# Optimization experiments

Hardware: AMD Instinct MI355X
Metric: run time of the kernel (lower is better)

Reference implementation:

```python
import jax, jax.numpy as jnp
import numpy as np

N = 200000   # nodes
E = 600000   # directed edges
G = 8192     # graphs in batch
D_IN = 30
H = 128


def setup_inputs() -> dict:
    key = jax.random.key(0)
    ks = jax.random.split(key, 9)
    x = jax.random.normal(ks[0], (N, D_IN), jnp.float32)
    edge_index = jax.random.randint(ks[1], (2, E), 0, N, dtype=jnp.int32)
    batch_idx = jnp.sort(jax.random.randint(ks[2], (N,), 0, G, dtype=jnp.int32))
    W1 = jax.random.normal(ks[3], (D_IN, H), jnp.float32) / np.sqrt(D_IN)
    b1 = jnp.zeros((H,), jnp.float32)
    W2 = jax.random.normal(ks[4], (H, H), jnp.float32) / np.sqrt(H)
    b2 = jnp.zeros((H,), jnp.float32)
    W3 = jax.random.normal(ks[5], (H, H), jnp.float32) / np.sqrt(H)
    b3 = jnp.zeros((H,), jnp.float32)
    return {"x": x, "edge_index": edge_index, "batch_idx": batch_idx,
            "W1": W1, "b1": b1, "W2": W2, "b2": b2, "W3": W3, "b3": b3}


def _gcn_layer(x, W, b, src, dst, dinv):
    h = x @ W                                   # [N, H]
    norm = (dinv[src] * dinv[dst])[:, None]     # per-edge normalization
    msg = h[src] * norm                         # [E, H] gather + scale
    agg = jax.ops.segment_sum(msg, dst, num_segments=N)
    agg = agg + h * (dinv * dinv)[:, None]      # self-loop term, norm = 1/deg
    return jax.nn.relu(agg + b)


def reference(x, edge_index, batch_idx, W1, b1, W2, b2, W3, b3):
    src, dst = edge_index[0], edge_index[1]
    # degree with self-loops (edge weight 1), aggregated at target (col)
    deg = 1.0 + jax.ops.segment_sum(jnp.ones((E,), x.dtype), dst, num_segments=N)
    dinv = jax.lax.rsqrt(deg)                   # deg >= 1, safe
    h = _gcn_layer(x, W1, b1, src, dst, dinv)
    h = _gcn_layer(h, W2, b2, src, dst, dinv)
    h = _gcn_layer(h, W3, b3, src, dst, dinv)
    # global mean pool over batch segments
    sums = jax.ops.segment_sum(h, batch_idx, num_segments=G)
    counts = jax.ops.segment_sum(jnp.ones((N,), h.dtype), batch_idx, num_segments=G)
    return sums / jnp.maximum(counts, 1.0)[:, None]
```

## Files before the change

kernel.cpp:

```cpp
#include <hip/hip_runtime.h>


#define DIN 30
#define HD  128

typedef __attribute__((ext_vector_type(8))) short v8s;
typedef __attribute__((ext_vector_type(4))) float v4f;

static __device__ __forceinline__ unsigned short f2bf(float f) {
  unsigned int u = __float_as_uint(f);
  u += 0x7fffu + ((u >> 16) & 1u);
  return (unsigned short)(u >> 16);
}
static __device__ __forceinline__ float bf2f(unsigned short s) {
  return __uint_as_float(((unsigned int)s) << 16);
}
static __device__ __forceinline__ float bflo(unsigned int u) {
  return __uint_as_float(u << 16);
}
static __device__ __forceinline__ float bfhi(unsigned int u) {
  return __uint_as_float(u & 0xffff0000u);
}

#define ACC8(v, s)                                            \
  {                                                           \
    a0 += (s) * (float)((v).x & 0xffu);                       \
    a1 += (s) * (float)(((v).x >> 8) & 0xffu);                \
    a2 += (s) * (float)(((v).x >> 16) & 0xffu);               \
    a3 += (s) * (float)((v).x >> 24);                         \
    a4 += (s) * (float)((v).y & 0xffu);                       \
    a5 += (s) * (float)(((v).y >> 8) & 0xffu);                \
    a6 += (s) * (float)(((v).y >> 16) & 0xffu);               \
    a7 += (s) * (float)((v).y >> 24);                         \
  }

__global__ void k_degree(const int* __restrict__ dst, int* __restrict__ deg,
                         int* __restrict__ eord, int E) {
  int e = blockIdx.x * blockDim.x + threadIdx.x;
  if (e < E) eord[e] = atomicAdd(&deg[dst[e]], 1);
}

__global__ void k_scan(const int* __restrict__ deg, int* __restrict__ scanbuf,
                       int* __restrict__ rowptr, float* __restrict__ dinv, int N) {
  __shared__ int s[256];
  __shared__ int sbase;
  int bid = blockIdx.x, tid = threadIdx.x;
  int base = bid * 1024 + tid * 4;
  int v[4]; int t = 0;
#pragma unroll
  for (int j = 0; j < 4; ++j) { int idx = base + j; v[j] = (idx < N) ? deg[idx] : 0; t += v[j]; }
  s[tid] = t; __syncthreads();
  for (int d = 1; d < 256; d <<= 1) {
    int u = (tid >= d) ? s[tid - d] : 0;
    __syncthreads();
    s[tid] += u;
    __syncthreads();
  }
  int myexcl = s[tid] - t;
  int blocktotal = s[255];
  if (tid == 0) atomicExch(&scanbuf[bid], blocktotal | 0x80000000);

  int pre = 0;
  for (int p = tid; p < bid; p += 256) {
    int val;
    do { val = atomicAdd(&scanbuf[p], 0); } while (!(val & 0x80000000));
    pre += val & 0x7fffffff;
  }
  __syncthreads();
  s[tid] = pre; __syncthreads();
  for (int d = 128; d > 0; d >>= 1) { if (tid < d) s[tid] += s[tid + d]; __syncthreads(); }
  if (tid == 0) sbase = s[0];
  __syncthreads();

  int run = sbase + myexcl;
#pragma unroll
  for (int j = 0; j < 4; ++j) {
    int idx = base + j;
    if (idx < N) {
      rowptr[idx] = run;
      dinv[idx] = rsqrtf((float)(1 + v[j]));
    }
    run += v[j];
    if (idx == N - 1) rowptr[N] = run;
  }
}

static __device__ __forceinline__ void wtf_one(const float* __restrict__ W,
                                               unsigned short* __restrict__ WTF,
                                               int idx, int Kreal, int KK) {
  int j = idx & 7;
  int c = idx >> 3;
  int l15 = c & 15;
  int quad = (c >> 4) & 3;
  int kk = (c >> 6) % KK;
  int t = c / (64 * KK);
  int k = kk * 32 + quad * 8 + j;
  int n = t * 16 + l15;
  WTF[idx] = (k < Kreal) ? f2bf(W[k * 128 + n]) : (unsigned short)0;
}

__global__ void k_prep(const int* __restrict__ src, const int* __restrict__ dst,
                       const int* __restrict__ rowptr, const int* __restrict__ eord,
                       int* __restrict__ col, int E,
                       const float* __restrict__ x, const float* __restrict__ dinv,
                       unsigned short* __restrict__ xb, int N,
                       const float* __restrict__ W1, const float* __restrict__ W2,
                       const float* __restrict__ W3,
                       unsigned short* __restrict__ W1F, unsigned short* __restrict__ W2F,
                       unsigned short* __restrict__ W3F,
                       const int* __restrict__ batch, int* __restrict__ gstart, int G,
                       float* __restrict__ out,
                       int SB, int XB, int WB, int BB) {
  int blk = blockIdx.x;
  if (blk < SB) {
    int e = blk * 256 + threadIdx.x;
    if (e < E) col[rowptr[dst[e]] + eord[e]] = src[e];
  } else if (blk < SB + XB) {
    int idx = (blk - SB) * 256 + threadIdx.x;
    if (idx < N * 32) {
      int n = idx >> 5, f = idx & 31;
      float v = (f < DIN) ? x[(size_t)n * DIN + f] * dinv[n] : 0.f;
      xb[idx] = f2bf(v);
    }
  } else if (blk < SB + XB + WB) {
    int idx = (blk - SB - XB) * 256 + threadIdx.x;
    if (idx < 4096) wtf_one(W1, W1F, idx, DIN, 1);
    else if (idx < 20480) wtf_one(W2, W2F, idx - 4096, 128, 4);
    else if (idx < 36864) wtf_one(W3, W3F, idx - 20480, 128, 4);
  } else if (blk < SB + XB + WB + BB) {
    int i = (blk - SB - XB - WB) * 256 + threadIdx.x;
    if (i >= N) return;
    int b = batch[i];
    int prev = (i == 0) ? -1 : batch[i - 1];
    for (int g = prev + 1; g <= b; ++g) gstart[g] = i;
    if (i == N - 1)
      for (int g = b + 1; g <= G; ++g) gstart[g] = N;
  } else {
    int idx = (blk - SB - XB - WB - BB) * 256 + threadIdx.x;
    if (idx < G * 32)
      ((float4*)out)[idx] = make_float4(0.f, 0.f, 0.f, 0.f);
  }
}

template <int K>
__global__ __launch_bounds__(1024, 8) void k_fused(const void* __restrict__ hin,
                                                   const float* __restrict__ hscale,
                                                   const unsigned short* __restrict__ WTF,
                                                   const float* __restrict__ b,
                                                   const int* __restrict__ rowptr,
                                                   const int* __restrict__ col,
                                                   const float* __restrict__ dinv,
                                                   unsigned char* __restrict__ Cq,
                                                   float* __restrict__ Cs, int N) {
  constexpr int KK = K / 32;
  constexpr int KP = (K == 128) ? 136 : 40;
  constexpr int CP = 132;
  constexpr int SMSZ = (64 * KP > 64 * CP) ? 64 * KP : 64 * CP;
  __shared__ __align__(16) unsigned short sm[SMSZ];

  int tid = threadIdx.x;
  int l16 = tid & 15;
  int nl = tid >> 4;
  int row0 = blockIdx.x * 64;
  int node = row0 + nl;

  if constexpr (K == 32) {
    const unsigned int* hp = (const unsigned int*)hin;
    float a0 = 0.f, a1 = 0.f;
    if (node < N) {
      unsigned int u = hp[(size_t)node * 16 + l16];
      a0 = bflo(u); a1 = bfhi(u);
      int e0 = rowptr[node], e1 = rowptr[node + 1];
      int e = e0;
      for (; e + 2 <= e1; e += 2) {
        int c0 = col[e], c1 = col[e + 1];
        unsigned int v0 = hp[(size_t)c0 * 16 + l16];
        unsigned int v1 = hp[(size_t)c1 * 16 + l16];
        a0 += bflo(v0); a1 += bfhi(v0);
        a0 += bflo(v1); a1 += bfhi(v1);
      }
      if (e < e1) {
        unsigned int v0 = hp[(size_t)col[e] * 16 + l16];
        a0 += bflo(v0); a1 += bfhi(v0);
      }
      float di = dinv[node];
      a0 *= di; a1 *= di;
    }
    *(unsigned int*)&sm[nl * KP + l16 * 2] =
        (unsigned int)f2bf(a0) | ((unsigned int)f2bf(a1) << 16);
  } else {
    const uint2* hq = (const uint2*)hin;
    float a0 = 0.f, a1 = 0.f, a2 = 0.f, a3 = 0.f, a4 = 0.f, a5 = 0.f, a6 = 0.f, a7 = 0.f;
    if (node < N) {
      uint2 u = hq[(size_t)node * 16 + l16];
      float ss = hscale[node];
      ACC8(u, ss);
      int e0 = rowptr[node], e1 = rowptr[node + 1];
      int e = e0;
      for (; e + 2 <= e1; e += 2) {
        int c0 = col[e], c1 = col[e + 1];
        uint2 v0 = hq[(size_t)c0 * 16 + l16];
        uint2 v1 = hq[(size_t)c1 * 16 + l16];
        float s0 = hscale[c0];
        float s1 = hscale[c1];
        ACC8(v0, s0);
        ACC8(v1, s1);
      }
      if (e < e1) {
        int c0 = col[e];
        uint2 v0 = hq[(size_t)c0 * 16 + l16];
        float s0 = hscale[c0];
        ACC8(v0, s0);
      }
      float di = dinv[node];
      a0 *= di; a1 *= di; a2 *= di; a3 *= di;
      a4 *= di; a5 *= di; a6 *= di; a7 *= di;
    }
    uint4 o;
    o.x = (unsigned int)f2bf(a0) | ((unsigned int)f2bf(a1) << 16);
    o.y = (unsigned int)f2bf(a2) | ((unsigned int)f2bf(a3) << 16);
    o.z = (unsigned int)f2bf(a4) | ((unsigned int)f2bf(a5) << 16);
    o.w = (unsigned int)f2bf(a6) | ((unsigned int)f2bf(a7) << 16);
    *(uint4*)&sm[nl * KP + l16 * 8] = o;
  }
  __syncthreads();

  int wv = tid >> 6, lane = tid & 63, quad = lane >> 4, l15 = lane & 15;
  int rt = wv & 3, tp = wv >> 2;
  v8s af[KK];
#pragma unroll
  for (int kk = 0; kk < KK; ++kk)
    af[kk] = *(const v8s*)&sm[(rt * 16 + l15) * KP + kk * 32 + quad * 8];
  __syncthreads();

  int crow0 = row0 + rt * 16 + quad * 4;
  float dr[4];
  if (crow0 + 3 < N) {
    float4 d4 = *(const float4*)&dinv[crow0];
    dr[0] = d4.x; dr[1] = d4.y; dr[2] = d4.z; dr[3] = d4.w;
  } else {
#pragma unroll
    for (int i = 0; i < 4; ++i) dr[i] = (crow0 + i < N) ? dinv[crow0 + i] : 0.f;
  }

#pragma unroll
  for (int tt = 0; tt < 2; ++tt) {
    int t = tp * 2 + tt;
    v4f acc = {0.f, 0.f, 0.f, 0.f};
#pragma unroll
    for (int kk = 0; kk < KK; ++kk) {
      v8s bf = *(const v8s*)(WTF + (size_t)(((t * KK + kk) * 4 + quad) * 16 + l15) * 8);
      acc = __builtin_amdgcn_mfma_f32_16x16x32_bf16(af[kk], bf, acc, 0, 0, 0);
    }
    float bias = b[t * 16 + l15];
#pragma unroll
    for (int i = 0; i < 4; ++i) {
      float o = fmaxf(acc[i] + bias, 0.f) * dr[i];
      sm[(rt * 16 + quad * 4 + i) * CP + t * 16 + l15] = f2bf(o);
    }
  }
  __syncthreads();

  {
    uint4 u = *(const uint4*)&sm[nl * CP + l16 * 8];
    float f0 = bflo(u.x), f1 = bfhi(u.x), f2 = bflo(u.y), f3 = bfhi(u.y);
    float f4 = bflo(u.z), f5 = bfhi(u.z), f6 = bflo(u.w), f7 = bfhi(u.w);
    float m = fmaxf(fmaxf(fmaxf(f0, f1), fmaxf(f2, f3)),
                    fmaxf(fmaxf(f4, f5), fmaxf(f6, f7)));
    m = fmaxf(m, __shfl_xor(m, 1));
    m = fmaxf(m, __shfl_xor(m, 2));
    m = fmaxf(m, __shfl_xor(m, 4));
    m = fmaxf(m, __shfl_xor(m, 8));
    float inv = (m > 0.f) ? 255.f / m : 0.f;
    unsigned q0 = (unsigned)__float2int_rn(fminf(f0 * inv, 255.f));
    unsigned q1 = (unsigned)__float2int_rn(fminf(f1 * inv, 255.f));
    unsigned q2 = (unsigned)__float2int_rn(fminf(f2 * inv, 255.f));
    unsigned q3 = (unsigned)__float2int_rn(fminf(f3 * inv, 255.f));
    unsigned q4 = (unsigned)__float2int_rn(fminf(f4 * inv, 255.f));
    unsigned q5 = (unsigned)__float2int_rn(fminf(f5 * inv, 255.f));
    unsigned q6 = (unsigned)__float2int_rn(fminf(f6 * inv, 255.f));
    unsigned q7 = (unsigned)__float2int_rn(fminf(f7 * inv, 255.f));
    uint2 o;
    o.x = q0 | (q1 << 8) | (q2 << 16) | (q3 << 24);
    o.y = q4 | (q5 << 8) | (q6 << 16) | (q7 << 24);
    int row = row0 + nl;
    if (row < N) {
      ((uint2*)Cq)[(size_t)row * 16 + l16] = o;
      if (l16 == 0) Cs[row] = m * (1.f / 255.f);
    }
  }
}

__global__ __launch_bounds__(1024, 8) void k_fused_pool(const unsigned char* __restrict__ hin,
                                                        const float* __restrict__ hscale,
                                                        const unsigned short* __restrict__ WTF,
                                                        const float* __restrict__ b,
                                                        const int* __restrict__ rowptr,
                                                        const int* __restrict__ col,
                                                        const float* __restrict__ dinv,
                                                        const int* __restrict__ batch,
                                                        float* __restrict__ out, int N) {
  constexpr int KK = 4, KP = 136, CP = 132;
  constexpr int SMSZ = 64 * KP;
  __shared__ __align__(16) unsigned short sm[SMSZ];
  __shared__ int sbatch[64];

  int tid = threadIdx.x;
  int l16 = tid & 15;
  int nl = tid >> 4;
  int row0 = blockIdx.x * 64;
  int node = row0 + nl;

  if (tid < 64) sbatch[tid] = (row0 + tid < N) ? batch[row0 + tid] : -1;

  {
    const uint2* hq = (const uint2*)hin;
    float a0 = 0.f, a1 = 0.f, a2 = 0.f, a3 = 0.f, a4 = 0.f, a5 = 0.f, a6 = 0.f, a7 = 0.f;
    if (node < N) {
      uint2 u = hq[(size_t)node * 16 + l16];
      float ss = hscale[node];
      ACC8(u, ss);
      int e0 = rowptr[node], e1 = rowptr[node + 1];
      int e = e0;
      for (; e + 2 <= e1; e += 2) {
        int c0 = col[e], c1 = col[e + 1];
        uint2 v0 = hq[(size_t)c0 * 16 + l16];
        uint2 v1 = hq[(size_t)c1 * 16 + l16];
        float s0 = hscale[c0];
        float s1 = hscale[c1];
        ACC8(v0, s0);
        ACC8(v1, s1);
      }
      if (e < e1) {
        int c0 = col[e];
        uint2 v0 = hq[(size_t)c0 * 16 + l16];
        float s0 = hscale[c0];
        ACC8(v0, s0);
      }
      float di = dinv[node];
      a0 *= di; a1 *= di; a2 *= di; a3 *= di;
      a4 *= di; a5 *= di; a6 *= di; a7 *= di;
    }
    uint4 o;
    o.x = (unsigned int)f2bf(a0) | ((unsigned int)f2bf(a1) << 16);
    o.y = (unsigned int)f2bf(a2) | ((unsigned int)f2bf(a3) << 16);
    o.z = (unsigned int)f2bf(a4) | ((unsigned int)f2bf(a5) << 16);
    o.w = (unsigned int)f2bf(a6) | ((unsigned int)f2bf(a7) << 16);
    *(uint4*)&sm[nl * KP + l16 * 8] = o;
  }
  __syncthreads();

  int wv = tid >> 6, lane = tid & 63, quad = lane >> 4, l15 = lane & 15;
  int rt = wv & 3, tp = wv >> 2;
  v8s af[KK];
#pragma unroll
  for (int kk = 0; kk < KK; ++kk)
    af[kk] = *(const v8s*)&sm[(rt * 16 + l15) * KP + kk * 32 + quad * 8];
  __syncthreads();

#pragma unroll
  for (int tt = 0; tt < 2; ++tt) {
    int t = tp * 2 + tt;
    v4f acc = {0.f, 0.f, 0.f, 0.f};
#pragma unroll
    for (int kk = 0; kk < KK; ++kk) {
      v8s bf = *(const v8s*)(WTF + (size_t)(((t * KK + kk) * 4 + quad) * 16 + l15) * 8);
      acc = __builtin_amdgcn_mfma_f32_16x16x32_bf16(af[kk], bf, acc, 0, 0, 0);
    }
    float bias = b[t * 16 + l15];
#pragma unroll
    for (int i = 0; i < 4; ++i) {
      float o = fmaxf(acc[i] + bias, 0.f);
      sm[(rt * 16 + quad * 4 + i) * CP + t * 16 + l15] = f2bf(o);
    }
  }
  __syncthreads();

  int f = tid & 127;
  int grp = tid >> 7;
  float run = 0.f;
  int cur = -1;
#pragma unroll
  for (int j = 0; j < 8; ++j) {
    int r = grp * 8 + j;
    int g = sbatch[r];
    if (g != cur) {
      if (cur >= 0) atomicAdd(&out[(size_t)cur * 128 + f], run);
      run = 0.f; cur = g;
    }
    if (g >= 0) run += bf2f(sm[r * CP + f]);
  }
  if (cur >= 0) atomicAdd(&out[(size_t)cur * 128 + f], run);
}

__global__ void k_finalize(float* __restrict__ out, const int* __restrict__ gstart, int G) {
  int idx = blockIdx.x * blockDim.x + threadIdx.x;
  if (idx >= G * 128) return;
  int g = idx >> 7;
  float cnt = (float)(gstart[g + 1] - gstart[g]);
  out[idx] = out[idx] / fmaxf(cnt, 1.f);
}

extern "C" void kernel_launch(void* const* d_in, const int* in_sizes, int n_in,
                              void* d_out, int out_size, void* d_ws, size_t ws_size,
                              hipStream_t stream) {
  const float* x  = (const float*)d_in[0];
  const int* ei   = (const int*)d_in[1];
  const int* batch = (const int*)d_in[2];
  const float* W1 = (const float*)d_in[3];
  const float* b1 = (const float*)d_in[4];
  const float* W2 = (const float*)d_in[5];
  const float* b2 = (const float*)d_in[6];
  const float* W3 = (const float*)d_in[7];
  const float* b3 = (const float*)d_in[8];
  float* out = (float*)d_out;
  int N = in_sizes[2];
  int E = in_sizes[1] / 2;
  int G = out_size / HD;
  const int* src = ei;
  const int* dst = ei + E;

  size_t off = 0;
  char* ws = (char*)d_ws;
  auto alloc = [&](size_t bytes) -> void* {
    void* p = ws + off;
    off += (bytes + 255) & ~(size_t)255;
    return p;
  };
  int nb1024 = (N + 1023) / 1024;
  int*   deg     = (int*)alloc((size_t)N * 4);
  int*   scanbuf = (int*)alloc((size_t)nb1024 * 4);
  float* dinv    = (float*)alloc((size_t)N * 4);
  int*   rowptr  = (int*)alloc((size_t)(N + 1) * 4);
  int*   eord    = (int*)alloc((size_t)E * 4);
  int*   col     = (int*)alloc((size_t)E * 4);
  int*   gstart  = (int*)alloc((size_t)(G + 1) * 4);
  unsigned short* xb  = (unsigned short*)alloc((size_t)N * 32 * 2);
  unsigned char*  hAq = (unsigned char*)alloc((size_t)N * 128);
  float*          hAs = (float*)alloc((size_t)N * 4);
  unsigned char*  hBq = (unsigned char*)alloc((size_t)N * 128);
  float*          hBs = (float*)alloc((size_t)N * 4);
  unsigned short* W1F = (unsigned short*)alloc(4096 * 2);
  unsigned short* W2F = (unsigned short*)alloc(16384 * 2);
  unsigned short* W3F = (unsigned short*)alloc(16384 * 2);
  (void)ws_size; (void)n_in;

  size_t zbytes = (size_t)((char*)dinv - (char*)deg);
  hipMemsetAsync(deg, 0, zbytes, stream);
  k_degree<<<(E + 255) / 256, 256, 0, stream>>>(dst, deg, eord, E);
  k_scan<<<nb1024, 256, 0, stream>>>(deg, scanbuf, rowptr, dinv, N);

  int SB = (E + 255) / 256;
  int XB = (N * 32 + 255) / 256;
  int WB = 144;
  int BB = (N + 255) / 256;
  int ZB = (G * 32 + 255) / 256;
  k_prep<<<SB + XB + WB + BB + ZB, 256, 0, stream>>>(src, dst, rowptr, eord, col, E,
                                                     x, dinv, xb, N,
                                                     W1, W2, W3, W1F, W2F, W3F,
                                                     batch, gstart, G, out,
                                                     SB, XB, WB, BB);

  int fusedBlocks = (N + 63) / 64;
  k_fused<32><<<fusedBlocks, 1024, 0, stream>>>(xb, nullptr, W1F, b1, rowptr, col, dinv,
                                                hAq, hAs, N);
  k_fused<128><<<fusedBlocks, 1024, 0, stream>>>(hAq, hAs, W2F, b2, rowptr, col, dinv,
                                                 hBq, hBs, N);
  k_fused_pool<<<fusedBlocks, 1024, 0, stream>>>(hBq, hBs, W3F, b3, rowptr, col, dinv,
                                                 batch, out, N);
  k_finalize<<<(G * 128 + 255) / 256, 256, 0, stream>>>(out, gstart, G);
}
```

Measured before the change: 295.1 us.

## Parallelize neighbor aggregation over block edges with LDS float atomics

Replaces the per-node serial CSR gather loop with a block-wide edge-parallel scheme. Each 64-node block walks its contiguous edge range 256 edges at a time and accumulates into an fp32 LDS tile with shared-memory atomics, using the local destination row packed into the top bits of col. The aim is to balance work across skewed degrees and raise memory-level parallelism. The cost is LDS atomic traffic, a larger fp32 shared tile that may lower occupancy, and the packing caps node ids at 18 bits (mask 0x3ffff = 262143), which only holds while N stays below that.

```diff
diff --git a/kernel.cpp b/kernel.cpp
--- a/kernel.cpp
+++ b/kernel.cpp
@@ -21,18 +21,6 @@
 static __device__ __forceinline__ float bfhi(unsigned int u) {
   return __uint_as_float(u & 0xffff0000u);
 }
-
-#define ACC8(v, s)                                            \
-  {                                                           \
-    a0 += (s) * (float)((v).x & 0xffu);                       \
-    a1 += (s) * (float)(((v).x >> 8) & 0xffu);                \
-    a2 += (s) * (float)(((v).x >> 16) & 0xffu);               \
-    a3 += (s) * (float)((v).x >> 24);                         \
-    a4 += (s) * (float)((v).y & 0xffu);                       \
-    a5 += (s) * (float)(((v).y >> 8) & 0xffu);                \
-    a6 += (s) * (float)(((v).y >> 16) & 0xffu);               \
-    a7 += (s) * (float)((v).y >> 24);                         \
-  }
 
 __global__ void k_degree(const int* __restrict__ dst, int* __restrict__ deg,
                          int* __restrict__ eord, int E) {
@@ -101,9 +89,9 @@
 
 __global__ void k_prep(const int* __restrict__ src, const int* __restrict__ dst,
                        const int* __restrict__ rowptr, const int* __restrict__ eord,
-                       int* __restrict__ col, int E,
+                       unsigned int* __restrict__ col, int E,
                        const float* __restrict__ x, const float* __restrict__ dinv,
-                       unsigned short* __restrict__ xb, int N,
+                       unsigned int* __restrict__ xb, int N,
                        const float* __restrict__ W1, const float* __restrict__ W2,
                        const float* __restrict__ W3,
                        unsigned short* __restrict__ W1F, unsigned short* __restrict__ W2F,
@@ -114,13 +102,18 @@
   int blk = blockIdx.x;
   if (blk < SB) {
     int e = blk * 256 + threadIdx.x;
-    if (e < E) col[rowptr[dst[e]] + eord[e]] = src[e];
+    if (e < E) {
+      int d = dst[e];
+      col[rowptr[d] + eord[e]] = (unsigned int)src[e] | ((unsigned int)(d & 63) << 26);
+    }
   } else if (blk < SB + XB) {
     int idx = (blk - SB) * 256 + threadIdx.x;
-    if (idx < N * 32) {
-      int n = idx >> 5, f = idx & 31;
-      float v = (f < DIN) ? x[(size_t)n * DIN + f] * dinv[n] : 0.f;
-      xb[idx] = f2bf(v);
+    if (idx < N * 16) {
+      int n = idx >> 4, w = idx & 15;
+      float di = dinv[n];
+      float v0 = x[(size_t)n * DIN + w] * di;
+      float v1 = (w + 16 < DIN) ? x[(size_t)n * DIN + w + 16] * di : 0.f;
+      xb[idx] = (unsigned int)f2bf(v0) | ((unsigned int)f2bf(v1) << 16);
     }
   } else if (blk < SB + XB + WB) {
     int idx = (blk - SB - XB) * 256 + threadIdx.x;
@@ -148,90 +141,124 @@
                                                    const unsigned short* __restrict__ WTF,
                                                    const float* __restrict__ b,
                                                    const int* __restrict__ rowptr,
-                                                   const int* __restrict__ col,
+                                                   const unsigned int* __restrict__ col,
                                                    const float* __restrict__ dinv,
                                                    unsigned char* __restrict__ Cq,
                                                    float* __restrict__ Cs, int N) {
   constexpr int KK = K / 32;
-  constexpr int KP = (K == 128) ? 136 : 40;
+  constexpr int AST = (K == 128) ? 132 : 36;
   constexpr int CP = 132;
-  constexpr int SMSZ = (64 * KP > 64 * CP) ? 64 * KP : 64 * CP;
-  __shared__ __align__(16) unsigned short sm[SMSZ];
+  constexpr int SMB = (64 * AST * 4 > 64 * CP * 2) ? 64 * AST * 4 : 64 * CP * 2;
+  __shared__ __align__(16) char smraw[SMB];
+  float* accf = (float*)smraw;
+  unsigned short* smc = (unsigned short*)smraw;
 
   int tid = threadIdx.x;
   int l16 = tid & 15;
-  int nl = tid >> 4;
+  int g = tid >> 4;
   int row0 = blockIdx.x * 64;
-  int node = row0 + nl;
+  int node = row0 + g;
 
   if constexpr (K == 32) {
-    const unsigned int* hp = (const unsigned int*)hin;
-    float a0 = 0.f, a1 = 0.f;
+    const unsigned int* xp = (const unsigned int*)hin;
     if (node < N) {
-      unsigned int u = hp[(size_t)node * 16 + l16];
-      a0 = bflo(u); a1 = bfhi(u);
-      int e0 = rowptr[node], e1 = rowptr[node + 1];
-      int e = e0;
-      for (; e + 2 <= e1; e += 2) {
-        int c0 = col[e], c1 = col[e + 1];
-        unsigned int v0 = hp[(size_t)c0 * 16 + l16];
-        unsigned int v1 = hp[(size_t)c1 * 16 + l16];
-        a0 += bflo(v0); a1 += bfhi(v0);
-        a0 += bflo(v1); a1 += bfhi(v1);
-      }
-      if (e < e1) {
-        unsigned int v0 = hp[(size_t)col[e] * 16 + l16];
-        a0 += bflo(v0); a1 += bfhi(v0);
-      }
-      float di = dinv[node];
-      a0 *= di; a1 *= di;
-    }
-    *(unsigned int*)&sm[nl * KP + l16 * 2] =
-        (unsigned int)f2bf(a0) | ((unsigned int)f2bf(a1) << 16);
+      unsigned int xw = xp[(size_t)node * 16 + l16];
+      accf[g * AST + l16]      = bflo(xw);
+      accf[g * AST + 16 + l16] = bfhi(xw);
+    } else {
+      accf[g * AST + l16]      = 0.f;
+      accf[g * AST + 16 + l16] = 0.f;
+    }
   } else {
     const uint2* hq = (const uint2*)hin;
-    float a0 = 0.f, a1 = 0.f, a2 = 0.f, a3 = 0.f, a4 = 0.f, a5 = 0.f, a6 = 0.f, a7 = 0.f;
     if (node < N) {
       uint2 u = hq[(size_t)node * 16 + l16];
-      float ss = hscale[node];
-      ACC8(u, ss);
-      int e0 = rowptr[node], e1 = rowptr[node + 1];
-      int e = e0;
-      for (; e + 2 <= e1; e += 2) {
-        int c0 = col[e], c1 = col[e + 1];
-        uint2 v0 = hq[(size_t)c0 * 16 + l16];
-        uint2 v1 = hq[(size_t)c1 * 16 + l16];
-        float s0 = hscale[c0];
-        float s1 = hscale[c1];
-        ACC8(v0, s0);
-        ACC8(v1, s1);
+      float s = hscale[node];
+      accf[g * AST + 0 * 16 + l16] = s * (float)(u.x & 0xffu);
+      accf[g * AST + 1 * 16 + l16] = s * (float)((u.x >> 8) & 0xffu);
+      accf[g * AST + 2 * 16 + l16] = s * (float)((u.x >> 16) & 0xffu);
+      accf[g * AST + 3 * 16 + l16] = s * (float)(u.x >> 24);
+      accf[g * AST + 4 * 16 + l16] = s * (float)(u.y & 0xffu);
+      accf[g * AST + 5 * 16 + l16] = s * (float)((u.y >> 8) & 0xffu);
+      accf[g * AST + 6 * 16 + l16] = s * (float)((u.y >> 16) & 0xffu);
+      accf[g * AST + 7 * 16 + l16] = s * (float)(u.y >> 24);
+    } else {
+#pragma unroll
+      for (int j = 0; j < 8; ++j) accf[g * AST + j * 16 + l16] = 0.f;
+    }
+  }
+  __syncthreads();
+
+  {
+    int rend = row0 + 64; if (rend > N) rend = N;
+    int eb = rowptr[row0];
+    int ee = rowptr[rend];
+    for (int b0 = eb; b0 < ee; b0 += 256) {
+      int e0 = b0 + g * 4;
+      unsigned int pc[4];
+      uint2 rv[4];
+      unsigned int xv[4];
+      float sc[4];
+#pragma unroll
+      for (int s = 0; s < 4; ++s) {
+        int e = e0 + s;
+        pc[s] = (e < ee) ? col[e] : 0xffffffffu;
       }
-      if (e < e1) {
-        int c0 = col[e];
-        uint2 v0 = hq[(size_t)c0 * 16 + l16];
-        float s0 = hscale[c0];
-        ACC8(v0, s0);
+#pragma unroll
+      for (int s = 0; s < 4; ++s) {
+        if (pc[s] != 0xffffffffu) {
+          unsigned int c = pc[s] & 0x3ffffu;
+          if constexpr (K == 32) {
+            xv[s] = ((const unsigned int*)hin)[(size_t)c * 16 + l16];
+          } else {
+            rv[s] = ((const uint2*)hin)[(size_t)c * 16 + l16];
+            sc[s] = hscale[c];
+          }
+        }
       }
-      float di = dinv[node];
-      a0 *= di; a1 *= di; a2 *= di; a3 *= di;
-      a4 *= di; a5 *= di; a6 *= di; a7 *= di;
-    }
-    uint4 o;
-    o.x = (unsigned int)f2bf(a0) | ((unsigned int)f2bf(a1) << 16);
-    o.y = (unsigned int)f2bf(a2) | ((unsigned int)f2bf(a3) << 16);
-    o.z = (unsigned int)f2bf(a4) | ((unsigned int)f2bf(a5) << 16);
-    o.w = (unsigned int)f2bf(a6) | ((unsigned int)f2bf(a7) << 16);
-    *(uint4*)&sm[nl * KP + l16 * 8] = o;
+#pragma unroll
+      for (int s = 0; s < 4; ++s) {
+        if (pc[s] != 0xffffffffu) {
+          int d = (int)(pc[s] >> 26);
+          if constexpr (K == 32) {
+            atomicAdd(&accf[d * AST + l16], bflo(xv[s]));
+            atomicAdd(&accf[d * AST + 16 + l16], bfhi(xv[s]));
+          } else {
+            float s0 = sc[s];
+            atomicAdd(&accf[d * AST + 0 * 16 + l16], s0 * (float)(rv[s].x & 0xffu));
+            atomicAdd(&accf[d * AST + 1 * 16 + l16], s0 * (float)((rv[s].x >> 8) & 0xffu));
+            atomicAdd(&accf[d * AST + 2 * 16 + l16], s0 * (float)((rv[s].x >> 16) & 0xffu));
+            atomicAdd(&accf[d * AST + 3 * 16 + l16], s0 * (float)(rv[s].x >> 24));
+            atomicAdd(&accf[d * AST + 4 * 16 + l16], s0 * (float)(rv[s].y & 0xffu));
+            atomicAdd(&accf[d * AST + 5 * 16 + l16], s0 * (float)((rv[s].y >> 8) & 0xffu));
+            atomicAdd(&accf[d * AST + 6 * 16 + l16], s0 * (float)((rv[s].y >> 16) & 0xffu));
+            atomicAdd(&accf[d * AST + 7 * 16 + l16], s0 * (float)(rv[s].y >> 24));
+          }
+        }
+      }
+    }
   }
   __syncthreads();
 
   int wv = tid >> 6, lane = tid & 63, quad = lane >> 4, l15 = lane & 15;
   int rt = wv & 3, tp = wv >> 2;
+  int arow = rt * 16 + l15;
+  float dn = (row0 + arow < N) ? dinv[row0 + arow] : 0.f;
   v8s af[KK];
 #pragma unroll
-  for (int kk = 0; kk < KK; ++kk)
-    af[kk] = *(const v8s*)&sm[(rt * 16 + l15) * KP + kk * 32 + quad * 8];
-  __syncthreads();
+  for (int kk = 0; kk < KK; ++kk) {
+    const float* p = &accf[arow * AST + kk * 32 + quad * 8];
+    float4 x0 = *(const float4*)p;
+    float4 x1 = *(const float4*)(p + 4);
+    af[kk][0] = (short)f2bf(x0.x * dn);
+    af[kk][1] = (short)f2bf(x0.y * dn);
+    af[kk][2] = (short)f2bf(x0.z * dn);
+    af[kk][3] = (short)f2bf(x0.w * dn);
+    af[kk][4] = (short)f2bf(x1.x * dn);
+    af[kk][5] = (short)f2bf(x1.y * dn);
+    af[kk][6] = (short)f2bf(x1.z * dn);
+    af[kk][7] = (short)f2bf(x1.w * dn);
+  }
 
   int crow0 = row0 + rt * 16 + quad * 4;
   float dr[4];
@@ -242,6 +269,7 @@
 #pragma unroll
     for (int i = 0; i < 4; ++i) dr[i] = (crow0 + i < N) ? dinv[crow0 + i] : 0.f;
   }
+  __syncthreads();
 
 #pragma unroll
   for (int tt = 0; tt < 2; ++tt) {
@@ -256,34 +284,30 @@
 #pragma unroll
     for (int i = 0; i < 4; ++i) {
       float o = fmaxf(acc[i] + bias, 0.f) * dr[i];
-      sm[(rt * 16 + quad * 4 + i) * CP + t * 16 + l15] = f2bf(o);
+      smc[(rt * 16 + quad * 4 + i) * CP + t * 16 + l15] = f2bf(o);
     }
   }
   __syncthreads();
 
   {
-    uint4 u = *(const uint4*)&sm[nl * CP + l16 * 8];
-    float f0 = bflo(u.x), f1 = bfhi(u.x), f2 = bflo(u.y), f3 = bfhi(u.y);
-    float f4 = bflo(u.z), f5 = bfhi(u.z), f6 = bflo(u.w), f7 = bfhi(u.w);
-    float m = fmaxf(fmaxf(fmaxf(f0, f1), fmaxf(f2, f3)),
-                    fmaxf(fmaxf(f4, f5), fmaxf(f6, f7)));
+    float f[8];
+#pragma unroll
+    for (int j = 0; j < 8; ++j) f[j] = bf2f(smc[g * CP + j * 16 + l16]);
+    float m = fmaxf(fmaxf(fmaxf(f[0], f[1]), fmaxf(f[2], f[3])),
+                    fmaxf(fmaxf(f[4], f[5]), fmaxf(f[6], f[7])));
     m = fmaxf(m, __shfl_xor(m, 1));
     m = fmaxf(m, __shfl_xor(m, 2));
     m = fmaxf(m, __shfl_xor(m, 4));
     m = fmaxf(m, __shfl_xor(m, 8));
     float inv = (m > 0.f) ? 255.f / m : 0.f;
-    unsigned q0 = (unsigned)__float2int_rn(fminf(f0 * inv, 255.f));
-    unsigned q1 = (unsigned)__float2int_rn(fminf(f1 * inv, 255.f));
-    unsigned q2 = (unsigned)__float2int_rn(fminf(f2 * inv, 255.f));
-    unsigned q3 = (unsigned)__float2int_rn(fminf(f3 * inv, 255.f));
-    unsigned q4 = (unsigned)__float2int_rn(fminf(f4 * inv, 255.f));
-    unsigned q5 = (unsigned)__float2int_rn(fminf(f5 * inv, 255.f));
-    unsigned q6 = (unsigned)__float2int_rn(fminf(f6 * inv, 255.f));
-    unsigned q7 = (unsigned)__float2int_rn(fminf(f7 * inv, 255.f));
+    unsigned q[8];
+#pragma unroll
+    for (int j = 0; j < 8; ++j)
+      q[j] = (unsigned)__float2int_rn(fminf(f[j] * inv, 255.f));
     uint2 o;
-    o.x = q0 | (q1 << 8) | (q2 << 16) | (q3 << 24);
-    o.y = q4 | (q5 << 8) | (q6 << 16) | (q7 << 24);
-    int row = row0 + nl;
+    o.x = q[0] | (q[1] << 8) | (q[2] << 16) | (q[3] << 24);
+    o.y = q[4] | (q[5] << 8) | (q[6] << 16) | (q[7] << 24);
+    int row = row0 + g;
     if (row < N) {
       ((uint2*)Cq)[(size_t)row * 16 + l16] = o;
       if (l16 == 0) Cs[row] = m * (1.f / 255.f);
@@ -296,66 +320,106 @@
                                                         const unsigned short* __restrict__ WTF,
                                                         const float* __restrict__ b,
                                                         const int* __restrict__ rowptr,
-                                                        const int* __restrict__ col,
+                                                        const unsigned int* __restrict__ col,
                                                         const float* __restrict__ dinv,
                                                         const int* __restrict__ batch,
                                                         float* __restrict__ out, int N) {
-  constexpr int KK = 4, KP = 136, CP = 132;
-  constexpr int SMSZ = 64 * KP;
-  __shared__ __align__(16) unsigned short sm[SMSZ];
+  constexpr int KK = 4, AST = 132, CP = 132;
+  constexpr int SMB = 64 * AST * 4;
+  __shared__ __align__(16) char smraw[SMB];
   __shared__ int sbatch[64];
+  float* accf = (float*)smraw;
+  unsigned short* smc = (unsigned short*)smraw;
 
   int tid = threadIdx.x;
   int l16 = tid & 15;
-  int nl = tid >> 4;
+  int g = tid >> 4;
   int row0 = blockIdx.x * 64;
-  int node = row0 + nl;
+  int node = row0 + g;
 
   if (tid < 64) sbatch[tid] = (row0 + tid < N) ? batch[row0 + tid] : -1;
 
   {
     const uint2* hq = (const uint2*)hin;
-    float a0 = 0.f, a1 = 0.f, a2 = 0.f, a3 = 0.f, a4 = 0.f, a5 = 0.f, a6 = 0.f, a7 = 0.f;
     if (node < N) {
       uint2 u = hq[(size_t)node * 16 + l16];
-      float ss = hscale[node];
-      ACC8(u, ss);
-      int e0 = rowptr[node], e1 = rowptr[node + 1];
-      int e = e0;
-      for (; e + 2 <= e1; e += 2) {
-        int c0 = col[e], c1 = col[e + 1];
-        uint2 v0 = hq[(size_t)c0 * 16 + l16];
-        uint2 v1 = hq[(size_t)c1 * 16 + l16];
-        float s0 = hscale[c0];
-        float s1 = hscale[c1];
-        ACC8(v0, s0);
-        ACC8(v1, s1);
+      float s = hscale[node];
+      accf[g * AST + 0 * 16 + l16] = s * (float)(u.x & 0xffu);
+      accf[g * AST + 1 * 16 + l16] = s * (float)((u.x >> 8) & 0xffu);
+      accf[g * AST + 2 * 16 + l16] = s * (float)((u.x >> 16) & 0xffu);
+      accf[g * AST + 3 * 16 + l16] = s * (float)(u.x >> 24);
+      accf[g * AST + 4 * 16 + l16] = s * (float)(u.y & 0xffu);
+      accf[g * AST + 5 * 16 + l16] = s * (float)((u.y >> 8) & 0xffu);
+      accf[g * AST + 6 * 16 + l16] = s * (float)((u.y >> 16) & 0xffu);
+      accf[g * AST + 7 * 16 + l16] = s * (float)(u.y >> 24);
+    } else {
+#pragma unroll
+      for (int j = 0; j < 8; ++j) accf[g * AST + j * 16 + l16] = 0.f;
+    }
+  }
+  __syncthreads();
+
+  {
+    int rend = row0 + 64; if (rend > N) rend = N;
+    int eb = rowptr[row0];
+    int ee = rowptr[rend];
+    const uint2* hq = (const uint2*)hin;
+    for (int b0 = eb; b0 < ee; b0 += 256) {
+      int e0 = b0 + g * 4;
+      unsigned int pc[4];
+      uint2 rv[4];
+      float sc[4];
+#pragma unroll
+      for (int s = 0; s < 4; ++s) {
+        int e = e0 + s;
+        pc[s] = (e < ee) ? col[e] : 0xffffffffu;
       }
-      if (e < e1) {
-        int c0 = col[e];
-        uint2 v0 = hq[(size_t)c0 * 16 + l16];
-        float s0 = hscale[c0];
-        ACC8(v0, s0);
+#pragma unroll
+      for (int s = 0; s < 4; ++s) {
+        if (pc[s] != 0xffffffffu) {
+          unsigned int c = pc[s] & 0x3ffffu;
+          rv[s] = hq[(size_t)c * 16 + l16];
+          sc[s] = hscale[c];
+        }
       }
-      float di = dinv[node];
-      a0 *= di; a1 *= di; a2 *= di; a3 *= di;
-      a4 *= di; a5 *= di; a6 *= di; a7 *= di;
-    }
-    uint4 o;
-    o.x = (unsigned int)f2bf(a0) | ((unsigned int)f2bf(a1) << 16);
-    o.y = (unsigned int)f2bf(a2) | ((unsigned int)f2bf(a3) << 16);
-    o.z = (unsigned int)f2bf(a4) | ((unsigned int)f2bf(a5) << 16);
-    o.w = (unsigned int)f2bf(a6) | ((unsigned int)f2bf(a7) << 16);
-    *(uint4*)&sm[nl * KP + l16 * 8] = o;
+#pragma unroll
+      for (int s = 0; s < 4; ++s) {
+        if (pc[s] != 0xffffffffu) {
+          int d = (int)(pc[s] >> 26);
+          float s0 = sc[s];
+          atomicAdd(&accf[d * AST + 0 * 16 + l16], s0 * (float)(rv[s].x & 0xffu));
+          atomicAdd(&accf[d * AST + 1 * 16 + l16], s0 * (float)((rv[s].x >> 8) & 0xffu));
+          atomicAdd(&accf[d * AST + 2 * 16 + l16], s0 * (float)((rv[s].x >> 16) & 0xffu));
+          atomicAdd(&accf[d * AST + 3 * 16 + l16], s0 * (float)(rv[s].x >> 24));
+          atomicAdd(&accf[d * AST + 4 * 16 + l16], s0 * (float)(rv[s].y & 0xffu));
+          atomicAdd(&accf[d * AST + 5 * 16 + l16], s0 * (float)((rv[s].y >> 8) & 0xffu));
+          atomicAdd(&accf[d * AST + 6 * 16 + l16], s0 * (float)((rv[s].y >> 16) & 0xffu));
+          atomicAdd(&accf[d * AST + 7 * 16 + l16], s0 * (float)(rv[s].y >> 24));
+        }
+      }
+    }
   }
   __syncthreads();
 
   int wv = tid >> 6, lane = tid & 63, quad = lane >> 4, l15 = lane & 15;
   int rt = wv & 3, tp = wv >> 2;
+  int arow = rt * 16 + l15;
+  float dn = (row0 + arow < N) ? dinv[row0 + arow] : 0.f;
   v8s af[KK];
 #pragma unroll
-  for (int kk = 0; kk < KK; ++kk)
-    af[kk] = *(const v8s*)&sm[(rt * 16 + l15) * KP + kk * 32 + quad * 8];
+  for (int kk = 0; kk < KK; ++kk) {
+    const float* p = &accf[arow * AST + kk * 32 + quad * 8];
+    float4 x0 = *(const float4*)p;
+    float4 x1 = *(const float4*)(p + 4);
+    af[kk][0] = (short)f2bf(x0.x * dn);
+    af[kk][1] = (short)f2bf(x0.y * dn);
+    af[kk][2] = (short)f2bf(x0.z * dn);
+    af[kk][3] = (short)f2bf(x0.w * dn);
+    af[kk][4] = (short)f2bf(x1.x * dn);
+    af[kk][5] = (short)f2bf(x1.y * dn);
+    af[kk][6] = (short)f2bf(x1.z * dn);
+    af[kk][7] = (short)f2bf(x1.w * dn);
+  }
   __syncthreads();
 
 #pragma unroll
@@ -371,7 +435,7 @@
 #pragma unroll
     for (int i = 0; i < 4; ++i) {
       float o = fmaxf(acc[i] + bias, 0.f);
-      sm[(rt * 16 + quad * 4 + i) * CP + t * 16 + l15] = f2bf(o);
+      smc[(rt * 16 + quad * 4 + i) * CP + t * 16 + l15] = f2bf(o);
     }
   }
   __syncthreads();
@@ -383,12 +447,12 @@
 #pragma unroll
   for (int j = 0; j < 8; ++j) {
     int r = grp * 8 + j;
-    int g = sbatch[r];
-    if (g != cur) {
+    int gg = sbatch[r];
+    if (gg != cur) {
       if (cur >= 0) atomicAdd(&out[(size_t)cur * 128 + f], run);
-      run = 0.f; cur = g;
-    }
-    if (g >= 0) run += bf2f(sm[r * CP + f]);
+      run = 0.f; cur = gg;
+    }
+    if (gg >= 0) run += bf2f(smc[r * CP + f]);
   }
   if (cur >= 0) atomicAdd(&out[(size_t)cur * 128 + f], run);
 }
@@ -433,9 +497,9 @@
   float* dinv    = (float*)alloc((size_t)N * 4);
   int*   rowptr  = (int*)alloc((size_t)(N + 1) * 4);
   int*   eord    = (int*)alloc((size_t)E * 4);
-  int*   col     = (int*)alloc((size_t)E * 4);
+  unsigned int* col = (unsigned int*)alloc((size_t)E * 4);
   int*   gstart  = (int*)alloc((size_t)(G + 1) * 4);
-  unsigned short* xb  = (unsigned short*)alloc((size_t)N * 32 * 2);
+  unsigned int*   xb  = (unsigned int*)alloc((size_t)N * 16 * 4);
   unsigned char*  hAq = (unsigned char*)alloc((size_t)N * 128);
   float*          hAs = (float*)alloc((size_t)N * 4);
   unsigned char*  hBq = (unsigned char*)alloc((size_t)N * 128);
@@ -451,7 +515,7 @@
   k_scan<<<nb1024, 256, 0, stream>>>(deg, scanbuf, rowptr, dinv, N);
 
   int SB = (E + 255) / 256;
-  int XB = (N * 32 + 255) / 256;
+  int XB = (N * 16 + 255) / 256;
   int WB = 144;
   int BB = (N + 255) / 256;
   int ZB = (G * 32 + 255) / 256;
```

Measured after the change: 1.138 ms. 3.86x slower.

## Stage neighbor rows cooperatively into LDS chunks before per-node aggregation

Applied to the files above, without the earlier changes.

Instead of each 16-lane group gathering its own node's neighbor rows directly from global memory, the whole block walks its contiguous CSR edge range in 256-edge chunks. It loads neighbor rows (and scales) into shared memory with wider, block-wide loads, then each node accumulates its slice from LDS. This balances gather work across the block regardless of degree skew and raises memory-level parallelism. The cost is two barriers per chunk and a large extra LDS allocation, which may reduce occupancy.

```diff
diff --git a/kernel.cpp b/kernel.cpp
--- a/kernel.cpp
+++ b/kernel.cpp
@@ -156,72 +156,96 @@
   constexpr int KP = (K == 128) ? 136 : 40;
   constexpr int CP = 132;
   constexpr int SMSZ = (64 * KP > 64 * CP) ? 64 * KP : 64 * CP;
+  constexpr int CH = 256;
+  constexpr int SST = (K == 128) ? 144 : 72;
   __shared__ __align__(16) unsigned short sm[SMSZ];
+  __shared__ __align__(16) unsigned char stg[CH * SST];
+  __shared__ float sscale[(K == 128) ? CH : 1];
 
   int tid = threadIdx.x;
   int l16 = tid & 15;
-  int nl = tid >> 4;
+  int g = tid >> 4;
   int row0 = blockIdx.x * 64;
-  int node = row0 + nl;
+  int node = row0 + g;
+  int rend = row0 + 64; if (rend > N) rend = N;
+
+  float a0 = 0.f, a1 = 0.f, a2 = 0.f, a3 = 0.f, a4 = 0.f, a5 = 0.f, a6 = 0.f, a7 = 0.f;
+  int e0 = 0, e1 = 0; float di = 0.f;
+  if (node < N) {
+    e0 = rowptr[node]; e1 = rowptr[node + 1]; di = dinv[node];
+    if constexpr (K == 32) {
+      unsigned int u = ((const unsigned int*)hin)[(size_t)node * 16 + l16];
+      a0 = bflo(u); a1 = bfhi(u);
+    } else {
+      uint2 u = ((const uint2*)hin)[(size_t)node * 16 + l16];
+      float s = hscale[node];
+      ACC8(u, s);
+    }
+  }
+  int eb = rowptr[row0];
+  int ee = rowptr[rend];
+
+  for (int c0 = eb; c0 < ee; c0 += CH) {
+#pragma unroll
+    for (int q = 0; q < (CH * 8) / 1024; ++q) {
+      int slot = q * 1024 + tid;
+      int eL = slot >> 3, l8 = slot & 7;
+      int e = c0 + eL;
+      if (e < ee) {
+        int c = col[e];
+        if constexpr (K == 32) {
+          uint2 v = ((const uint2*)hin)[(size_t)c * 8 + l8];
+          *(uint2*)&stg[eL * SST + l8 * 8] = v;
+        } else {
+          uint4 v = ((const uint4*)hin)[(size_t)c * 8 + l8];
+          *(uint4*)&stg[eL * SST + l8 * 16] = v;
+          if (l8 == 0) sscale[eL] = hscale[c];
+        }
+      }
+    }
+    __syncthreads();
+    int lo = (e0 > c0) ? e0 : c0;
+    int hi = (e1 < c0 + CH) ? e1 : (c0 + CH);
+    int e2 = lo;
+    for (; e2 + 2 <= hi; e2 += 2) {
+      int i0 = e2 - c0, i1 = i0 + 1;
+      if constexpr (K == 32) {
+        unsigned int w0 = *(const unsigned int*)&stg[i0 * SST + l16 * 4];
+        unsigned int w1 = *(const unsigned int*)&stg[i1 * SST + l16 * 4];
+        a0 += bflo(w0); a1 += bfhi(w0);
+        a0 += bflo(w1); a1 += bfhi(w1);
+      } else {
+        uint2 w0 = *(const uint2*)&stg[i0 * SST + l16 * 8];
+        uint2 w1 = *(const uint2*)&stg[i1 * SST + l16 * 8];
+        float s0 = sscale[i0], s1 = sscale[i1];
+        ACC8(w0, s0);
+        ACC8(w1, s1);
+      }
+    }
+    if (e2 < hi) {
+      int i0 = e2 - c0;
+      if constexpr (K == 32) {
+        unsigned int w0 = *(const unsigned int*)&stg[i0 * SST + l16 * 4];
+        a0 += bflo(w0); a1 += bfhi(w0);
+      } else {
+        uint2 w0 = *(const uint2*)&stg[i0 * SST + l16 * 8];
+        float s0 = sscale[i0];
+        ACC8(w0, s0);
+      }
+    }
+    __syncthreads();
+  }
 
   if constexpr (K == 32) {
-    const unsigned int* hp = (const unsigned int*)hin;
-    float a0 = 0.f, a1 = 0.f;
-    if (node < N) {
-      unsigned int u = hp[(size_t)node * 16 + l16];
-      a0 = bflo(u); a1 = bfhi(u);
-      int e0 = rowptr[node], e1 = rowptr[node + 1];
-      int e = e0;
-      for (; e + 2 <= e1; e += 2) {
-        int c0 = col[e], c1 = col[e + 1];
-        unsigned int v0 = hp[(size_t)c0 * 16 + l16];
-        unsigned int v1 = hp[(size_t)c1 * 16 + l16];
-        a0 += bflo(v0); a1 += bfhi(v0);
-        a0 += bflo(v1); a1 += bfhi(v1);
-      }
-      if (e < e1) {
-        unsigned int v0 = hp[(size_t)col[e] * 16 + l16];
-        a0 += bflo(v0); a1 += bfhi(v0);
-      }
-      float di = dinv[node];
-      a0 *= di; a1 *= di;
-    }
-    *(unsigned int*)&sm[nl * KP + l16 * 2] =
-        (unsigned int)f2bf(a0) | ((unsigned int)f2bf(a1) << 16);
+    *(unsigned int*)&sm[g * KP + l16 * 2] =
+        (unsigned int)f2bf(a0 * di) | ((unsigned int)f2bf(a1 * di) << 16);
   } else {
-    const uint2* hq = (const uint2*)hin;
-    float a0 = 0.f, a1 = 0.f, a2 = 0.f, a3 = 0.f, a4 = 0.f, a5 = 0.f, a6 = 0.f, a7 = 0.f;
-    if (node < N) {
-      uint2 u = hq[(size_t)node * 16 + l16];
-      float ss = hscale[node];
-      ACC8(u, ss);
-      int e0 = rowptr[node], e1 = rowptr[node + 1];
-      int e = e0;
-      for (; e + 2 <= e1; e += 2) {
-        int c0 = col[e], c1 = col[e + 1];
-        uint2 v0 = hq[(size_t)c0 * 16 + l16];
-        uint2 v1 = hq[(size_t)c1 * 16 + l16];
-        float s0 = hscale[c0];
-        float s1 = hscale[c1];
-        ACC8(v0, s0);
-        ACC8(v1, s1);
-      }
-      if (e < e1) {
-        int c0 = col[e];
-        uint2 v0 = hq[(size_t)c0 * 16 + l16];
-        float s0 = hscale[c0];
-        ACC8(v0, s0);
-      }
-      float di = dinv[node];
-      a0 *= di; a1 *= di; a2 *= di; a3 *= di;
-      a4 *= di; a5 *= di; a6 *= di; a7 *= di;
-    }
     uint4 o;
-    o.x = (unsigned int)f2bf(a0) | ((unsigned int)f2bf(a1) << 16);
-    o.y = (unsigned int)f2bf(a2) | ((unsigned int)f2bf(a3) << 16);
-    o.z = (unsigned int)f2bf(a4) | ((unsigned int)f2bf(a5) << 16);
-    o.w = (unsigned int)f2bf(a6) | ((unsigned int)f2bf(a7) << 16);
-    *(uint4*)&sm[nl * KP + l16 * 8] = o;
+    o.x = (unsigned int)f2bf(a0 * di) | ((unsigned int)f2bf(a1 * di) << 16);
+    o.y = (unsigned int)f2bf(a2 * di) | ((unsigned int)f2bf(a3 * di) << 16);
+    o.z = (unsigned int)f2bf(a4 * di) | ((unsigned int)f2bf(a5 * di) << 16);
+    o.w = (unsigned int)f2bf(a6 * di) | ((unsigned int)f2bf(a7 * di) << 16);
+    *(uint4*)&sm[g * KP + l16 * 8] = o;
   }
   __syncthreads();
 
@@ -262,7 +286,7 @@
   __syncthreads();
 
   {
-    uint4 u = *(const uint4*)&sm[nl * CP + l16 * 8];
+    uint4 u = *(const uint4*)&sm[g * CP + l16 * 8];
     float f0 = bflo(u.x), f1 = bfhi(u.x), f2 = bflo(u.y), f3 = bfhi(u.y);
     float f4 = bflo(u.z), f5 = bfhi(u.z), f6 = bflo(u.w), f7 = bfhi(u.w);
     float m = fmaxf(fmaxf(fmaxf(f0, f1), fmaxf(f2, f3)),
@@ -283,7 +307,7 @@
     uint2 o;
     o.x = q0 | (q1 << 8) | (q2 << 16) | (q3 << 24);
     o.y = q4 | (q5 << 8) | (q6 << 16) | (q7 << 24);
-    int row = row0 + nl;
+    int row = row0 + g;
     if (row < N) {
       ((uint2*)Cq)[(size_t)row * 16 + l16] = o;
       if (l16 == 0) Cs[row] = m * (1.f / 255.f);
@@ -302,51 +326,73 @@
                                                         float* __restrict__ out, int N) {
   constexpr int KK = 4, KP = 136, CP = 132;
   constexpr int SMSZ = 64 * KP;
+  constexpr int CH = 256, SST = 144;
   __shared__ __align__(16) unsigned short sm[SMSZ];
+  __shared__ __align__(16) unsigned char stg[CH * SST];
+  __shared__ float sscale[CH];
   __shared__ int sbatch[64];
 
   int tid = threadIdx.x;
   int l16 = tid & 15;
-  int nl = tid >> 4;
+  int g = tid >> 4;
   int row0 = blockIdx.x * 64;
-  int node = row0 + nl;
+  int node = row0 + g;
+  int rend = row0 + 64; if (rend > N) rend = N;
 
   if (tid < 64) sbatch[tid] = (row0 + tid < N) ? batch[row0 + tid] : -1;
 
+  float a0 = 0.f, a1 = 0.f, a2 = 0.f, a3 = 0.f, a4 = 0.f, a5 = 0.f, a6 = 0.f, a7 = 0.f;
+  int e0 = 0, e1 = 0; float di = 0.f;
+  if (node < N) {
+    e0 = rowptr[node]; e1 = rowptr[node + 1]; di = dinv[node];
+    uint2 u = ((const uint2*)hin)[(size_t)node * 16 + l16];
+    float s = hscale[node];
+    ACC8(u, s);
+  }
+  int eb = rowptr[row0];
+  int ee = rowptr[rend];
+
+  for (int c0 = eb; c0 < ee; c0 += CH) {
+#pragma unroll
+    for (int q = 0; q < 2; ++q) {
+      int slot = q * 1024 + tid;
+      int eL = slot >> 3, l8 = slot & 7;
+      int e = c0 + eL;
+      if (e < ee) {
+        int c = col[e];
+        uint4 v = ((const uint4*)hin)[(size_t)c * 8 + l8];
+        *(uint4*)&stg[eL * SST + l8 * 16] = v;
+        if (l8 == 0) sscale[eL] = hscale[c];
+      }
+    }
+    __syncthreads();
+    int lo = (e0 > c0) ? e0 : c0;
+    int hi = (e1 < c0 + CH) ? e1 : (c0 + CH);
+    int e2 = lo;
+    for (; e2 + 2 <= hi; e2 += 2) {
+      int i0 = e2 - c0, i1 = i0 + 1;
+      uint2 w0 = *(const uint2*)&stg[i0 * SST + l16 * 8];
+      uint2 w1 = *(const uint2*)&stg[i1 * SST + l16 * 8];
+      float s0 = sscale[i0], s1 = sscale[i1];
+      ACC8(w0, s0);
+      ACC8(w1, s1);
+    }
+    if (e2 < hi) {
+      int i0 = e2 - c0;
+      uint2 w0 = *(const uint2*)&stg[i0 * SST + l16 * 8];
+      float s0 = sscale[i0];
+      ACC8(w0, s0);
+    }
+    __syncthreads();
+  }
+
   {
-    const uint2* hq = (const uint2*)hin;
-    float a0 = 0.f, a1 = 0.f, a2 = 0.f, a3 = 0.f, a4 = 0.f, a5 = 0.f, a6 = 0.f, a7 = 0.f;
-    if (node < N) {
-      uint2 u = hq[(size_t)node * 16 + l16];
-      float ss = hscale[node];
-      ACC8(u, ss);
-      int e0 = rowptr[node], e1 = rowptr[node + 1];
-      int e = e0;
-      for (; e + 2 <= e1; e += 2) {
-        int c0 = col[e], c1 = col[e + 1];
-        uint2 v0 = hq[(size_t)c0 * 16 + l16];
-        uint2 v1 = hq[(size_t)c1 * 16 + l16];
-        float s0 = hscale[c0];
-        float s1 = hscale[c1];
-        ACC8(v0, s0);
-        ACC8(v1, s1);
-      }
-      if (e < e1) {
-        int c0 = col[e];
-        uint2 v0 = hq[(size_t)c0 * 16 + l16];
-        float s0 = hscale[c0];
-        ACC8(v0, s0);
-      }
-      float di = dinv[node];
-      a0 *= di; a1 *= di; a2 *= di; a3 *= di;
-      a4 *= di; a5 *= di; a6 *= di; a7 *= di;
-    }
     uint4 o;
-    o.x = (unsigned int)f2bf(a0) | ((unsigned int)f2bf(a1) << 16);
-    o.y = (unsigned int)f2bf(a2) | ((unsigned int)f2bf(a3) << 16);
-    o.z = (unsigned int)f2bf(a4) | ((unsigned int)f2bf(a5) << 16);
-    o.w = (unsigned int)f2bf(a6) | ((unsigned int)f2bf(a7) << 16);
-    *(uint4*)&sm[nl * KP + l16 * 8] = o;
+    o.x = (unsigned int)f2bf(a0 * di) | ((unsigned int)f2bf(a1 * di) << 16);
+    o.y = (unsigned int)f2bf(a2 * di) | ((unsigned int)f2bf(a3 * di) << 16);
+    o.z = (unsigned int)f2bf(a4 * di) | ((unsigned int)f2bf(a5 * di) << 16);
+    o.w = (unsigned int)f2bf(a6 * di) | ((unsigned int)f2bf(a7 * di) << 16);
+    *(uint4*)&sm[g * KP + l16 * 8] = o;
   }
   __syncthreads();
 
@@ -383,12 +429,12 @@
 #pragma unroll
   for (int j = 0; j < 8; ++j) {
     int r = grp * 8 + j;
-    int g = sbatch[r];
-    if (g != cur) {
+    int gg = sbatch[r];
+    if (gg != cur) {
       if (cur >= 0) atomicAdd(&out[(size_t)cur * 128 + f], run);
-      run = 0.f; cur = g;
-    }
-    if (g >= 0) run += bf2f(sm[r * CP + f]);
+      run = 0.f; cur = gg;
+    }
+    if (gg >= 0) run += bf2f(sm[r * CP + f]);
   }
   if (cur >= 0) atomicAdd(&out[(size_t)cur * 128 + f], run);
 }
```

Result: faster. 286.0 us (-3.1%).
